# Optimization experiments

Measured on AMD Instinct MI355X. Metric: run time of the kernel, lower is better.

## Reference

```python
import jax, jax.numpy as jnp
import numpy as np

DIM = 1024

def setup_inputs() -> dict:
    key = jax.random.key(0)
    k1, k2, k3, k4 = jax.random.split(key, 4)
    x = jax.random.normal(k1, (4, 4096, DIM), dtype=jnp.float32)
    A = jax.random.normal(k2, (DIM, DIM), dtype=jnp.float32) * 0.01
    B_w = jax.random.normal(k3, (DIM, DIM), dtype=jnp.float32) * (1.0 / np.sqrt(DIM))
    C_w = jax.random.normal(k4, (DIM, DIM), dtype=jnp.float32) * (1.0 / np.sqrt(DIM))
    D = jnp.ones((DIM,), dtype=jnp.float32)
    return {"x": x, "A": A, "B_w": B_w, "C_w": C_w, "D": D}

def reference(x, A, B_w, C_w, D):
    # x: [B, L, Dm]; recurrence: h_t = tanh(h_{t-1} @ A.T + x_t @ B_w.T)
    #                 y_t = h_t @ C_w.T + D * x_t
    Bsz, L, Dm = x.shape
    # Precompute the input projection for all steps at once (one big GEMM).
    bx = jnp.einsum('bld,ed->ble', x, B_w)  # [B, L, Dm]

    def step(h, inputs):
        bx_t, x_t = inputs
        h = jnp.tanh(h @ A.T + bx_t)
        y = h @ C_w.T + D * x_t
        return h, y

    h0 = jnp.zeros((Bsz, Dm), dtype=x.dtype)
    # scan over time axis: move L to leading dim
    _, ys = jax.lax.scan(step, h0, (jnp.swapaxes(bx, 0, 1), jnp.swapaxes(x, 0, 1)))
    return jnp.swapaxes(ys, 0, 1)  # [B, L, Dm]
```

## Files before the change

kernel.cpp:

```cpp
#include <hip/hip_runtime.h>
#include <math.h>

#define DM   1024
#define BSZ  4
#define LSEQ 4096
#define GPB  32
#define RPW  32
#define TPB  512
#define SEGC 64
#define SSP  68
#define HSW2 1088

typedef unsigned long long u64;

__global__ __launch_bounds__(256) void bx_gemm_kernel(
    const float* __restrict__ X, const float* __restrict__ Bw,
    float* __restrict__ out)
{
    __shared__ float xs[16][68];
    __shared__ float bs[16][68];
    const int bm = blockIdx.x, bn = blockIdx.y;
    const int t  = threadIdx.x;
    const int tx = t & 15, ty = t >> 4;
    const int ml = t >> 2;
    const int kq = (t & 3) * 4;
    const float* xg = X  + (size_t)(bm * 64 + ml) * DM + kq;
    const float* bg = Bw + (size_t)(bn * 64 + ml) * DM + kq;
    float acc[4][4] = {};
    for (int k0 = 0; k0 < DM; k0 += 16) {
        float4 xv = *(const float4*)(xg + k0);
        float4 bv = *(const float4*)(bg + k0);
        __syncthreads();
        xs[kq+0][ml] = xv.x; xs[kq+1][ml] = xv.y; xs[kq+2][ml] = xv.z; xs[kq+3][ml] = xv.w;
        bs[kq+0][ml] = bv.x; bs[kq+1][ml] = bv.y; bs[kq+2][ml] = bv.z; bs[kq+3][ml] = bv.w;
        __syncthreads();
        #pragma unroll
        for (int kk = 0; kk < 16; ++kk) {
            float a[4], c[4];
            #pragma unroll
            for (int i = 0; i < 4; ++i) a[i] = xs[kk][ty*4+i];
            #pragma unroll
            for (int j = 0; j < 4; ++j) c[j] = bs[kk][tx*4+j];
            #pragma unroll
            for (int i = 0; i < 4; ++i)
                #pragma unroll
                for (int j = 0; j < 4; ++j)
                    acc[i][j] += a[i] * c[j];
        }
    }
    #pragma unroll
    for (int i = 0; i < 4; ++i) {
        float4 v = make_float4(acc[i][0], acc[i][1], acc[i][2], acc[i][3]);
        *(float4*)(out + (size_t)(bm*64 + ty*4 + i)*DM + bn*64 + tx*4) = v;
    }
}

__device__ __forceinline__ u64 poll_word(u64* fast, u64* safe, unsigned tag,
                                         u64 v, int& fastok)
{
    if ((unsigned)(v >> 32) == tag) return v;
    if (fastok) {
        #pragma unroll 1
        for (int i = 0; i < 16; ++i) {
            v = __hip_atomic_fetch_add(fast, 0ULL, __ATOMIC_RELAXED,
                                       __HIP_MEMORY_SCOPE_WORKGROUP);
            if ((unsigned)(v >> 32) == tag) return v;
        }
    }
    int spins = 0;
    do {
        v = __hip_atomic_load(safe, __ATOMIC_RELAXED, __HIP_MEMORY_SCOPE_AGENT);
    } while ((unsigned)(v >> 32) != tag && ++spins < (1 << 20));
    if (fastok) {
        u64 f = __hip_atomic_fetch_add(fast, 0ULL, __ATOMIC_RELAXED,
                                       __HIP_MEMORY_SCOPE_WORKGROUP);
        if ((unsigned)(f >> 32) != tag) fastok = 0;
    }
    return v;
}

__device__ __forceinline__ float fast_tanh(float x)
{
    float e = __expf(2.0f * x);
    return (e - 1.0f) / (e + 1.0f);
}

__global__ __launch_bounds__(TPB, 2) void scan_kernel(
    const float* __restrict__ A, const float* __restrict__ Cw,
    const float* __restrict__ Dv, const float* __restrict__ X,
    float* __restrict__ Y, u64* hfast, u64* hsafe)
{
    const int r = blockIdx.x & 7;
    if (r >= BSZ) return;
    const int b  = r;
    const int gw = blockIdx.x >> 3;
    const int r0 = gw * RPW;

    __shared__ float hs0[2 * HSW2];
    const int t   = threadIdx.x;
    const int row = t >> 4;
    const int seg = t & 15;
    const bool lead = (seg == 0);

    float ra[SEGC], rc[SEGC];
    {
        const float* Ap = A  + (size_t)(r0 + row) * DM + seg * SEGC;
        const float* Cp = Cw + (size_t)(r0 + row) * DM + seg * SEGC;
        #pragma unroll
        for (int u = 0; u < SEGC / 4; ++u) {
            float4 v = *(const float4*)(Ap + u*4);
            ra[u*4+0]=v.x; ra[u*4+1]=v.y; ra[u*4+2]=v.z; ra[u*4+3]=v.w;
            float4 w = *(const float4*)(Cp + u*4);
            rc[u*4+0]=w.x; rc[u*4+1]=w.y; rc[u*4+2]=w.z; rc[u*4+3]=w.w;
        }
    }
    const float dv = Dv[r0 + row];

    const int c0 = t, c1 = t + 512;
    const int s0 = (c0 >> 6) * SSP + (c0 & 63);
    const int s1 = (c1 >> 6) * SSP + (c1 & 63);
    int fastok = 1;

    u64 v0 = __hip_atomic_load(hsafe + (size_t)b * DM + c0, __ATOMIC_RELAXED, __HIP_MEMORY_SCOPE_AGENT);
    u64 v1 = __hip_atomic_load(hsafe + (size_t)b * DM + c1, __ATOMIC_RELAXED, __HIP_MEMORY_SCOPE_AGENT);
    float bxv = 0.f;
    float xv  = 0.f;
    if (lead) bxv = Y[(size_t)b*LSEQ*DM + r0 + row];

    for (int k = 0; k <= LSEQ; ++k) {
        const unsigned tag = (unsigned)k;
        const size_t slot = (size_t)(k & 1) * BSZ * DM + (size_t)b * DM;
        int dummy = 0;
        int& fo = (k == 0) ? dummy : fastok;

        v0 = poll_word(hfast + slot + c0, hsafe + slot + c0, tag, v0, fo);
        v1 = poll_word(hfast + slot + c1, hsafe + slot + c1, tag, v1, fo);

        float* hsk = hs0 + (k & 1) * HSW2;
        hsk[s0] = __uint_as_float((unsigned)v0);
        hsk[s1] = __uint_as_float((unsigned)v1);
        __syncthreads();

        float accA = 0.f, accC = 0.f;
        {
            const float4* h4p = (const float4*)(hsk + seg * SSP);
            #pragma unroll
            for (int u = 0; u < SEGC / 4; ++u) {
                float4 h4 = h4p[u];
                accA += ra[u*4+0]*h4.x + ra[u*4+1]*h4.y + ra[u*4+2]*h4.z + ra[u*4+3]*h4.w;
                accC += rc[u*4+0]*h4.x + rc[u*4+1]*h4.y + rc[u*4+2]*h4.z + rc[u*4+3]*h4.w;
            }
        }

        float xv_next = xv;
        if (k < LSEQ) {
            accA += __shfl_xor(accA, 1);
            accA += __shfl_xor(accA, 2);
            accA += __shfl_xor(accA, 4);
            accA += __shfl_xor(accA, 8);
            const size_t nslot = (size_t)((k+1) & 1) * BSZ * DM + (size_t)b * DM;
            if (lead) {
                float hv = fast_tanh(accA + bxv);
                u64 pk = ((u64)(unsigned)(k + 1) << 32) | (u64)__float_as_uint(hv);
                __hip_atomic_store(hfast + nslot + r0 + row, pk,
                                   __ATOMIC_RELAXED, __HIP_MEMORY_SCOPE_WORKGROUP);
                __hip_atomic_store(hsafe + nslot + r0 + row, pk,
                                   __ATOMIC_RELAXED, __HIP_MEMORY_SCOPE_AGENT);
            }
            if (fastok) {
                v0 = __hip_atomic_fetch_add(hfast + nslot + c0, 0ULL,
                                            __ATOMIC_RELAXED, __HIP_MEMORY_SCOPE_WORKGROUP);
                v1 = __hip_atomic_fetch_add(hfast + nslot + c1, 0ULL,
                                            __ATOMIC_RELAXED, __HIP_MEMORY_SCOPE_WORKGROUP);
            } else {
                v0 = __hip_atomic_load(hsafe + nslot + c0, __ATOMIC_RELAXED, __HIP_MEMORY_SCOPE_AGENT);
                v1 = __hip_atomic_load(hsafe + nslot + c1, __ATOMIC_RELAXED, __HIP_MEMORY_SCOPE_AGENT);
            }
            if (lead) {
                xv_next = X[(size_t)b*LSEQ*DM + (size_t)k*DM + r0 + row];
                if (k + 1 < LSEQ)
                    bxv = Y[(size_t)b*LSEQ*DM + (size_t)(k+1)*DM + r0 + row];
            }
        }

        if (k > 0) {
            accC += __shfl_xor(accC, 1);
            accC += __shfl_xor(accC, 2);
            accC += __shfl_xor(accC, 4);
            accC += __shfl_xor(accC, 8);
            if (lead) {
                const size_t yoff = (size_t)b*LSEQ*DM + (size_t)(k-1)*DM + r0 + row;
                Y[yoff] = accC + dv * xv;
            }
        }
        xv = xv_next;
    }
}

extern "C" void kernel_launch(void* const* d_in, const int* in_sizes, int n_in,
                              void* d_out, int out_size, void* d_ws, size_t ws_size,
                              hipStream_t stream)
{
    const float* X  = (const float*)d_in[0];
    const float* A  = (const float*)d_in[1];
    const float* Bw = (const float*)d_in[2];
    const float* Cw = (const float*)d_in[3];
    const float* Dv = (const float*)d_in[4];
    float* Y    = (float*)d_out;
    u64* hfast  = (u64*)d_ws;
    u64* hsafe  = hfast + (size_t)2 * BSZ * DM;

    hipMemsetAsync(d_ws, 0, (size_t)4 * BSZ * DM * sizeof(u64), stream);

    dim3 g1((BSZ * LSEQ) / 64, DM / 64);
    bx_gemm_kernel<<<g1, 256, 0, stream>>>(X, Bw, Y);
    scan_kernel<<<256, TPB, 0, stream>>>(A, Cw, Dv, X, Y, hfast, hsafe);
}
```

Measured before the change: 11.42 ms.

## Use 1024-thread blocks, one h word per thread, L2-only polling loads

The scan kernel grows to 1024 threads per block, so each thread owns one element of h and a 32-element segment of its row. The reduction gains one more shuffle stage and register use per thread roughly halves. Polling of the fast copy switches from atomic fetch_add to inline-asm global loads with the sc0 cache bit, and the next-step prefetch moves to the end of the iteration. The barrier is replaced by a raw s_waitcnt plus s_barrier. These changes aim to cut the per-step cost of cross-block synchronisation and LDS staging on the serial recurrence, at the risk of breaking memory-model guarantees and changing occupancy.

Result: slower. 14.94 ms (+30.8%).

```diff
diff --git a/kernel.cpp b/kernel.cpp
--- a/kernel.cpp
+++ b/kernel.cpp
@@ -6,8 +6,8 @@
 #define LSEQ 4096
 #define GPB  32
 #define RPW  32
-#define TPB  512
-#define SEGC 64
+#define TPB  1024
+#define SEGC 32
 #define SSP  68
 #define HSW2 1088
 
@@ -55,27 +55,14 @@
     }
 }
 
-__device__ __forceinline__ u64 poll_word(u64* fast, u64* safe, unsigned tag,
-                                         u64 v, int& fastok)
-{
-    if ((unsigned)(v >> 32) == tag) return v;
-    if (fastok) {
-        #pragma unroll 1
-        for (int i = 0; i < 16; ++i) {
-            v = __hip_atomic_fetch_add(fast, 0ULL, __ATOMIC_RELAXED,
-                                       __HIP_MEMORY_SCOPE_WORKGROUP);
-            if ((unsigned)(v >> 32) == tag) return v;
-        }
-    }
-    int spins = 0;
-    do {
-        v = __hip_atomic_load(safe, __ATOMIC_RELAXED, __HIP_MEMORY_SCOPE_AGENT);
-    } while ((unsigned)(v >> 32) != tag && ++spins < (1 << 20));
-    if (fastok) {
-        u64 f = __hip_atomic_fetch_add(fast, 0ULL, __ATOMIC_RELAXED,
-                                       __HIP_MEMORY_SCOPE_WORKGROUP);
-        if ((unsigned)(f >> 32) != tag) fastok = 0;
-    }
+__device__ __forceinline__ unsigned tg(u64 v) { return (unsigned)(v >> 32); }
+
+__device__ __forceinline__ u64 l2_load(const u64* p)
+{
+    u64 v;
+    asm volatile("global_load_dwordx2 %0, %1, off sc0\n\t"
+                 "s_waitcnt vmcnt(0)"
+                 : "=v"(v) : "v"(p) : "memory");
     return v;
 }
 
@@ -85,7 +72,7 @@
     return (e - 1.0f) / (e + 1.0f);
 }
 
-__global__ __launch_bounds__(TPB, 2) void scan_kernel(
+__global__ __launch_bounds__(TPB, 4) void scan_kernel(
     const float* __restrict__ A, const float* __restrict__ Cw,
     const float* __restrict__ Dv, const float* __restrict__ X,
     float* __restrict__ Y, u64* hfast, u64* hsafe)
@@ -98,8 +85,8 @@
 
     __shared__ float hs0[2 * HSW2];
     const int t   = threadIdx.x;
-    const int row = t >> 4;
-    const int seg = t & 15;
+    const int row = t >> 5;
+    const int seg = t & 31;
     const bool lead = (seg == 0);
 
     float ra[SEGC], rc[SEGC];
@@ -116,13 +103,13 @@
     }
     const float dv = Dv[r0 + row];
 
-    const int c0 = t, c1 = t + 512;
-    const int s0 = (c0 >> 6) * SSP + (c0 & 63);
-    const int s1 = (c1 >> 6) * SSP + (c1 & 63);
+    const int c0 = t;
+    const int s0 = (t >> 6) * SSP + (t & 63);
+    const int hb = (seg >> 1) * SSP + (seg & 1) * 32;
     int fastok = 1;
 
-    u64 v0 = __hip_atomic_load(hsafe + (size_t)b * DM + c0, __ATOMIC_RELAXED, __HIP_MEMORY_SCOPE_AGENT);
-    u64 v1 = __hip_atomic_load(hsafe + (size_t)b * DM + c1, __ATOMIC_RELAXED, __HIP_MEMORY_SCOPE_AGENT);
+    u64 v0 = __hip_atomic_load(hsafe + (size_t)b * DM + c0, __ATOMIC_RELAXED,
+                               __HIP_MEMORY_SCOPE_AGENT);
     float bxv = 0.f;
     float xv  = 0.f;
     if (lead) bxv = Y[(size_t)b*LSEQ*DM + r0 + row];
@@ -130,20 +117,36 @@
     for (int k = 0; k <= LSEQ; ++k) {
         const unsigned tag = (unsigned)k;
         const size_t slot = (size_t)(k & 1) * BSZ * DM + (size_t)b * DM;
-        int dummy = 0;
-        int& fo = (k == 0) ? dummy : fastok;
-
-        v0 = poll_word(hfast + slot + c0, hsafe + slot + c0, tag, v0, fo);
-        v1 = poll_word(hfast + slot + c1, hsafe + slot + c1, tag, v1, fo);
+
+        if (tg(v0) != tag) {
+            if (k == 0 || !fastok) {
+                int spins = 0;
+                do {
+                    v0 = __hip_atomic_load(hsafe + slot + c0, __ATOMIC_RELAXED,
+                                           __HIP_MEMORY_SCOPE_AGENT);
+                } while (tg(v0) != tag && ++spins < (1 << 20));
+            } else {
+                int i = 0;
+                while (tg(v0) != tag && i < 64) { v0 = l2_load(hfast + slot + c0); ++i; }
+                if (tg(v0) != tag) {
+                    int spins = 0;
+                    do {
+                        v0 = __hip_atomic_load(hsafe + slot + c0, __ATOMIC_RELAXED,
+                                               __HIP_MEMORY_SCOPE_AGENT);
+                    } while (tg(v0) != tag && ++spins < (1 << 20));
+                    u64 f = l2_load(hfast + slot + c0);
+                    if (tg(f) != tag) fastok = 0;
+                }
+            }
+        }
 
         float* hsk = hs0 + (k & 1) * HSW2;
         hsk[s0] = __uint_as_float((unsigned)v0);
-        hsk[s1] = __uint_as_float((unsigned)v1);
-        __syncthreads();
+        asm volatile("s_waitcnt lgkmcnt(0)\n\ts_barrier" ::: "memory");
 
         float accA = 0.f, accC = 0.f;
         {
-            const float4* h4p = (const float4*)(hsk + seg * SSP);
+            const float4* h4p = (const float4*)(hsk + hb);
             #pragma unroll
             for (int u = 0; u < SEGC / 4; ++u) {
                 float4 h4 = h4p[u];
@@ -153,12 +156,13 @@
         }
 
         float xv_next = xv;
+        const size_t nslot = (size_t)((k+1) & 1) * BSZ * DM + (size_t)b * DM;
         if (k < LSEQ) {
             accA += __shfl_xor(accA, 1);
             accA += __shfl_xor(accA, 2);
             accA += __shfl_xor(accA, 4);
             accA += __shfl_xor(accA, 8);
-            const size_t nslot = (size_t)((k+1) & 1) * BSZ * DM + (size_t)b * DM;
+            accA += __shfl_xor(accA, 16);
             if (lead) {
                 float hv = fast_tanh(accA + bxv);
                 u64 pk = ((u64)(unsigned)(k + 1) << 32) | (u64)__float_as_uint(hv);
@@ -167,15 +171,6 @@
                 __hip_atomic_store(hsafe + nslot + r0 + row, pk,
                                    __ATOMIC_RELAXED, __HIP_MEMORY_SCOPE_AGENT);
             }
-            if (fastok) {
-                v0 = __hip_atomic_fetch_add(hfast + nslot + c0, 0ULL,
-                                            __ATOMIC_RELAXED, __HIP_MEMORY_SCOPE_WORKGROUP);
-                v1 = __hip_atomic_fetch_add(hfast + nslot + c1, 0ULL,
-                                            __ATOMIC_RELAXED, __HIP_MEMORY_SCOPE_WORKGROUP);
-            } else {
-                v0 = __hip_atomic_load(hsafe + nslot + c0, __ATOMIC_RELAXED, __HIP_MEMORY_SCOPE_AGENT);
-                v1 = __hip_atomic_load(hsafe + nslot + c1, __ATOMIC_RELAXED, __HIP_MEMORY_SCOPE_AGENT);
-            }
             if (lead) {
                 xv_next = X[(size_t)b*LSEQ*DM + (size_t)k*DM + r0 + row];
                 if (k + 1 < LSEQ)
@@ -188,12 +183,19 @@
             accC += __shfl_xor(accC, 2);
             accC += __shfl_xor(accC, 4);
             accC += __shfl_xor(accC, 8);
+            accC += __shfl_xor(accC, 16);
             if (lead) {
                 const size_t yoff = (size_t)b*LSEQ*DM + (size_t)(k-1)*DM + r0 + row;
                 Y[yoff] = accC + dv * xv;
             }
         }
         xv = xv_next;
+
+        if (k < LSEQ) {
+            if (fastok) v0 = l2_load(hfast + nslot + c0);
+            else        v0 = __hip_atomic_load(hsafe + nslot + c0, __ATOMIC_RELAXED,
+                                               __HIP_MEMORY_SCOPE_AGENT);
+        }
     }
 }
 
```
